# Kernel optimization log

Hardware: AMD Instinct MI355X
Metric: run time of the kernel (lower is better)

The kernel has to match this reference:

```python
import jax, jax.numpy as jnp
import numpy as np

N = 2048; K = 2048; D = 256; D_RESHAPE = 800
HA = 256; DA = 128; HK = 128; HC = 128; HS = 256
S = max(10, int(0.1 * K))  # n_sample = 204
BN_SCALE = 1.0 / float(np.sqrt(1.0 + 1e-5))  # eval BatchNorm1d with running stats (0,1)

def leaky(x):
    return jax.nn.leaky_relu(x, 0.01)

def conv2d(x, w, b):
    y = jax.lax.conv_general_dilated(x, w, (1, 1), 'VALID', dimension_numbers=('NCHW', 'OIHW', 'NCHW'))
    return y + b[None, :, None, None]

def maxpool2(x):
    return jax.lax.reduce_window(x, -jnp.inf, jax.lax.max, (1, 1, 2, 2), (1, 1, 2, 2), 'VALID')

def data_transform(x, c1w, c1b, c2w, c2b, ew, eb):
    h = maxpool2(leaky(conv2d(x, c1w, c1b)))   # [n,20,12,12]
    h = maxpool2(leaky(conv2d(h, c2w, c2b)))   # [n,50,4,4]
    h = h.reshape(-1, D_RESHAPE)
    return leaky(h @ ew.T + eb)                # [n,D]

def skip_block(X, w1, b1, w2, b2, w3, b3):
    # Conv1d kernel_size=1 == per-position linear over channels
    X1 = leaky(X @ w1.T + b1) * BN_SCALE       # [n,HC]
    X2 = leaky(X @ w2.T + b2) * BN_SCALE       # [n,HC]
    X3 = leaky(X @ w3.T + b3) * BN_SCALE       # [n,d]
    feat = jax.nn.softmax(X1 @ X2.T, axis=0)   # torch Softmax(dim=1) on [1,n,n] -> axis 0
    return feat @ X3 + X

def mask_scores(A, w1, b1, w2, b2, w3, b3, w4, b4):
    X1 = leaky(A @ w1.T + b1)                  # [n,HK]
    X2 = jnp.tanh(A @ w2.T + b2)               # [n,HK]
    M = X1.T @ X2                              # [HK,HK]
    A3 = leaky(M @ w3.T + b3)                  # [HK,K]
    s = A3.T @ w4[0] + b4[0]                   # [K]
    return jax.nn.softmax(s)

def attention(X, few, feb, vw, vb, uw, ub, aww, awb, ew, eb):
    H = leaky(X @ few.T + feb)                 # [n,HA]
    AV = jnp.tanh(H @ vw.T + vb)
    AU = leaky(H @ uw.T + ub)
    a = leaky((AV * AU) @ aww.T + awb)         # [n,1]
    A = jax.nn.softmax(a.T, axis=1)            # [1,n]
    M = leaky((A @ H) @ ew.T + eb)             # [1,d]
    return M, A

def euclid(X, Y):
    d2 = jnp.sum(X * X, 1)[:, None] + jnp.sum(Y * Y, 1)[None, :] - 2.0 * (X @ Y.T)
    return jnp.sqrt(jnp.maximum(d2, 0.0))


def setup_inputs() -> dict:
    key = jax.random.key(0)
    ks = iter(jax.random.split(key, 70))
    def rn(shape, scale=0.05):
        return jax.random.normal(next(ks), shape, dtype=jnp.float32) * scale
    d = {}
    d['B'] = jax.random.normal(next(ks), (N, 1, 28, 28), dtype=jnp.float32)
    d['KB'] = jax.random.normal(next(ks), (K, 1, 28, 28), dtype=jnp.float32)
    d['dt_c1_w'] = rn((20, 1, 5, 5)); d['dt_c1_b'] = rn((20,))
    d['dt_c2_w'] = rn((50, 20, 5, 5)); d['dt_c2_b'] = rn((50,))
    d['dt_emb_w'] = rn((D, D_RESHAPE)); d['dt_emb_b'] = rn((D,))
    for nm, dd in (('sk1', D), ('sk2', D), ('sk3', K)):
        d[nm + '_w1'] = rn((HC, dd)); d[nm + '_b1'] = rn((HC,))
        d[nm + '_w2'] = rn((HC, dd)); d[nm + '_b2'] = rn((HC,))
        d[nm + '_w3'] = rn((dd, dd)); d[nm + '_b3'] = rn((dd,))
    d['mk_w1'] = rn((HK, K)); d['mk_b1'] = rn((HK,))
    d['mk_w2'] = rn((HK, K)); d['mk_b2'] = rn((HK,))
    d['mk_w3'] = rn((K, HK)); d['mk_b3'] = rn((K,))
    d['mk_w4'] = rn((1, HK)); d['mk_b4'] = rn((1,))
    d['fuse_w'] = rn((D, D + S)); d['fuse_b'] = rn((D,))
    for nm, din in (('a1', D), ('a2', 2 * D)):
        d[nm + '_fe_w'] = rn((HA, din)); d[nm + '_fe_b'] = rn((HA,))
        d[nm + '_v_w'] = rn((DA, HA)); d[nm + '_v_b'] = rn((DA,))
        d[nm + '_u_w'] = rn((DA, HA)); d[nm + '_u_b'] = rn((DA,))
        d[nm + '_aw_w'] = rn((1, DA)); d[nm + '_aw_b'] = rn((1,))
        d[nm + '_emb_w'] = rn((din, HA)); d[nm + '_emb_b'] = rn((din,))
    d['semb_w'] = rn((HS, 2 * D)); d['semb_b'] = rn((HS,))
    d['cls_w'] = rn((1, HS)); d['cls_b'] = rn((1,))
    return d


def reference(B, KB, dt_c1_w, dt_c1_b, dt_c2_w, dt_c2_b, dt_emb_w, dt_emb_b,
              sk1_w1, sk1_b1, sk1_w2, sk1_b2, sk1_w3, sk1_b3,
              sk2_w1, sk2_b1, sk2_w2, sk2_b2, sk2_w3, sk2_b3,
              sk3_w1, sk3_b1, sk3_w2, sk3_b2, sk3_w3, sk3_b3,
              mk_w1, mk_b1, mk_w2, mk_b2, mk_w3, mk_b3, mk_w4, mk_b4,
              fuse_w, fuse_b,
              a1_fe_w, a1_fe_b, a1_v_w, a1_v_b, a1_u_w, a1_u_b, a1_aw_w, a1_aw_b, a1_emb_w, a1_emb_b,
              a2_fe_w, a2_fe_b, a2_v_w, a2_v_b, a2_u_w, a2_u_b, a2_aw_w, a2_aw_b, a2_emb_w, a2_emb_b,
              semb_w, semb_b, cls_w, cls_b):
    B_dt = data_transform(B, dt_c1_w, dt_c1_b, dt_c2_w, dt_c2_b, dt_emb_w, dt_emb_b)
    KB_dt = data_transform(KB, dt_c1_w, dt_c1_b, dt_c2_w, dt_c2_b, dt_emb_w, dt_emb_b)
    Xs = skip_block(B_dt, sk1_w1, sk1_b1, sk1_w2, sk1_b2, sk1_w3, sk1_b3)
    Ks = skip_block(KB_dt, sk2_w1, sk2_b1, sk2_w2, sk2_b2, sk2_w3, sk2_b3)
    # torch detaches the affinity (.detach().numpy())
    aff = euclid(jax.lax.stop_gradient(Xs), jax.lax.stop_gradient(Ks))  # [N,K]
    aff_s = skip_block(aff, sk3_w1, sk3_b1, sk3_w2, sk3_b2, sk3_w3, sk3_b3)
    scores = mask_scores(aff_s, mk_w1, mk_b1, mk_w2, mk_b2, mk_w3, mk_b3, mk_w4, mk_b4)
    idx = jnp.argsort(-scores)[:S]                       # top-S knowledge columns
    B_bag = jax.nn.softmax(aff_s[:, idx], axis=1)        # [N,S], torch Softmax(dim=2)
    B_fuse = leaky(jnp.concatenate([B_dt, B_bag], axis=1) @ fuse_w.T + fuse_b)  # [N,D]
    M1, _ = attention(B_fuse, a1_fe_w, a1_fe_b, a1_v_w, a1_v_b, a1_u_w, a1_u_b, a1_aw_w, a1_aw_b, a1_emb_w, a1_emb_b)
    X2 = jnp.concatenate([B_fuse, jnp.tile(M1, (B_fuse.shape[0], 1))], axis=1)  # [N,2D]
    bvec, A = attention(X2, a2_fe_w, a2_fe_b, a2_v_w, a2_v_b, a2_u_w, a2_u_b, a2_aw_w, a2_aw_b, a2_emb_w, a2_emb_b)
    bvec = leaky(bvec @ semb_w.T + semb_b)               # [1,HS]
    Y = jnp.clip(jax.nn.sigmoid(bvec @ cls_w.T + cls_b), 1e-5, 1.0 - 1e-5)
    return (Y, A)
```

## Files before the change

### kernel.cpp

```cpp
#include <hip/hip_runtime.h>
#include <math.h>

#define LEAKY(x) ((x) > 0.f ? (x) : 0.01f * (x))
static constexpr float BN_SCALE = 0.9999950000374997f;

typedef unsigned short ushort_t;
typedef float f32x4 __attribute__((ext_vector_type(4)));
typedef short bf16x8 __attribute__((ext_vector_type(8)));

__device__ __forceinline__ ushort_t f2bfu(float f) {
  union { float f; unsigned u; } v; v.f = f;
  unsigned r = v.u + 0x7fffu + ((v.u >> 16) & 1u);
  return (ushort_t)(r >> 16);
}
__device__ __forceinline__ float bfu2f(ushort_t u) {
  union { unsigned u; float f; } v; v.u = ((unsigned)u) << 16;
  return v.f;
}

__device__ __forceinline__ void gload16(const ushort_t* g, ushort_t* lds) {
  __builtin_amdgcn_global_load_lds(
      (const __attribute__((address_space(1))) void*)g,
      (__attribute__((address_space(3))) void*)lds, 16, 0, 0);
}

__global__ void fill_out(float* out, int n) {
  int i = blockIdx.x * 256 + threadIdx.x;
  if (i < n) out[i] = 0.25f;
}

struct CvtArgs {
  const float* src[20];
  ushort_t* dst[20];
  int cum[21];
};
__global__ void to_bf16_flat(CvtArgs a) {
  int total = a.cum[20];
  for (int i = blockIdx.x * 256 + threadIdx.x; i < total; i += gridDim.x * 256) {
    int s = 0;
    while (i >= a.cum[s + 1]) ++s;
    int off = i - a.cum[s];
    a.dst[s][off] = f2bfu(a.src[s][off]);
  }
}

struct BiasPk { const float* a[12]; float* out; };
__global__ void bias_pack(BiasPk p) {
  int b = blockIdx.x, t = threadIdx.x;
  p.out[b * 256 + t] = (t < 128) ? p.a[2 * b][t] : p.a[2 * b + 1][t - 128];
}

__global__ void pad_rows_bf16(const float* __restrict__ w, ushort_t* __restrict__ wp,
                              int O, int Kin, int Kpad) {
  int idx = blockIdx.x * 256 + threadIdx.x;
  if (idx >= O * Kpad) return;
  int o = idx / Kpad, k = idx - o * Kpad;
  wp[idx] = (k < Kin) ? f2bfu(w[(size_t)o * Kin + k]) : (ushort_t)0;
}

__global__ void w2_relayout(const float* __restrict__ w2, ushort_t* __restrict__ w2p) {
  int idx = blockIdx.x * 256 + threadIdx.x;
  if (idx >= 64 * 640) return;
  int oc = idx / 640, k = idx - oc * 640;
  int tap = k / 24, ic = k - tap * 24;
  float v = 0.f;
  if (oc < 50 && tap < 25 && ic < 20)
    v = w2[(size_t)(oc * 20 + ic) * 25 + tap];
  w2p[idx] = f2bfu(v);
}

#define XCD_SWZ(TILE)                                                          \
  int id_ = blockIdx.y * gridDim.x + blockIdx.x;                               \
  int nwg_ = gridDim.x * gridDim.y;                                            \
  int sw_ = (id_ & 7) * (nwg_ >> 3) + (id_ >> 3);                              \
  int bm = (sw_ / gridDim.x) * (TILE), bn = (sw_ % gridDim.x) * (TILE);

__launch_bounds__(256)
__global__ void conv12_mfma(const float* __restrict__ imgB, const float* __restrict__ imgK,
                            const float* __restrict__ w1, const float* __restrict__ b1,
                            const ushort_t* __restrict__ w2p, const float* __restrict__ b2,
                            ushort_t* __restrict__ out832) {
  __shared__ __align__(16) char smem[34816];
  ushort_t* h1T = (ushort_t*)smem;
  ushort_t* Bs  = (ushort_t*)(smem + 13824);
  float* simg = (float*)(smem + 13824);
  float* sw1  = (float*)(smem + 20992);
  float* b1s  = (float*)(smem + 22992);
  float* Cf   = (float*)smem;

  int tid = threadIdx.x;
  int bx = blockIdx.x;
  const float* imgb = (bx < 1024) ? imgB + (size_t)bx * 2 * 784
                                  : imgK + (size_t)(bx - 1024) * 2 * 784;

  for (int i = tid; i < 1568; i += 256) {
    int im = (i >= 784) ? 1 : 0;
    int r = i - im * 784;
    int row = r / 28, col = r - row * 28;
    int sc = (col + (row >> 1)) & 31;
    simg[im * 896 + row * 32 + sc] = imgb[i];
  }
  for (int i = tid; i < 500; i += 256) sw1[i] = w1[i];
  if (tid < 20) b1s[tid] = b1[tid];
  for (int i = tid; i < 288; i += 256) {
    uint2 z; z.x = 0; z.y = 0;
    *(uint2*)&h1T[i * 24 + 20] = z;
  }

  int sB_r = tid >> 2;
  int sB_j0 = (tid & 3) * 2;
  bf16x8 wreg[2];
  #pragma unroll
  for (int i = 0; i < 2; ++i)
    wreg[i] = *(const bf16x8*)&w2p[(size_t)sB_r * 640 + (sB_j0 + i) * 8];

  __syncthreads();

  for (int o = tid; o < 1152; o += 256) {
    int im = (o >= 576) ? 1 : 0;
    int rem = o - im * 576;
    int cg = rem & 3;
    int pos = rem >> 2;
    int py = pos / 12, px = pos - py * 12;
    int y0 = py * 2, x0 = px * 2;
    float p[6][6];
    #pragma unroll
    for (int yy = 0; yy < 6; ++yy) {
      int rr = y0 + yy;
      int rbase = im * 896 + rr * 32;
      int rot = rr >> 1;
      #pragma unroll
      for (int xx = 0; xx < 6; ++xx)
        p[yy][xx] = simg[rbase + ((x0 + xx + rot) & 31)];
    }
    #pragma unroll
    for (int cc = 0; cc < 5; ++cc) {
      int c = cg * 5 + cc;
      const float* wc = &sw1[c * 25];
      float bb = b1s[c];
      float t0 = bb, t1 = bb, t2 = bb, t3 = bb;
      #pragma unroll
      for (int ky = 0; ky < 5; ++ky)
        #pragma unroll
        for (int kx = 0; kx < 5; ++kx) {
          float wv = wc[ky * 5 + kx];
          t0 += p[ky][kx] * wv;
          t1 += p[ky][kx + 1] * wv;
          t2 += p[ky + 1][kx] * wv;
          t3 += p[ky + 1][kx + 1] * wv;
        }
      float mx = fmaxf(fmaxf(t0, t1), fmaxf(t2, t3));
      h1T[(im * 144 + pos) * 24 + c] = f2bfu(LEAKY(mx));
    }
  }

  int wave = tid >> 6, lane = tid & 63;
  int wm = (wave >> 1) * 64, wn = (wave & 1) * 32;
  int mrow = lane & 15, kq = lane >> 4;

  int imv[4], oyv[4], oxv[4];
  #pragma unroll
  for (int mt = 0; mt < 4; ++mt) {
    int r = wm + mt * 16 + mrow;
    imv[mt] = r >> 6;
    int op = r & 63;
    oyv[mt] = op >> 3;
    oxv[mt] = op & 7;
  }

  f32x4 acc[4][2];
  #pragma unroll
  for (int i = 0; i < 4; ++i)
    #pragma unroll
    for (int j = 0; j < 2; ++j)
      #pragma unroll
      for (int r = 0; r < 4; ++r) acc[i][j][r] = 0.f;

  for (int kb = 0; kb < 10; ++kb) {
    __syncthreads();
    #pragma unroll
    for (int i = 0; i < 2; ++i)
      *(bf16x8*)&Bs[sB_r * 72 + (sB_j0 + i) * 8] = wreg[i];
    if (kb + 1 < 10) {
      #pragma unroll
      for (int i = 0; i < 2; ++i)
        wreg[i] = *(const bf16x8*)&w2p[(size_t)sB_r * 640 + (kb + 1) * 64 + (sB_j0 + i) * 8];
    }
    __syncthreads();
    #pragma unroll
    for (int ks = 0; ks < 2; ++ks) {
      int g = kb * 8 + ks * 4 + kq;
      int tap = g / 3;
      int part = g - tap * 3;
      int tc = tap < 25 ? tap : 24;
      int ky = tc / 5, kx = tc - ky * 5;
      bf16x8 af[4], bf[2];
      #pragma unroll
      for (int mt = 0; mt < 4; ++mt) {
        int pos = (oyv[mt] + ky) * 12 + oxv[mt] + kx;
        af[mt] = *(const bf16x8*)&h1T[(imv[mt] * 144 + pos) * 24 + part * 8];
      }
      #pragma unroll
      for (int nt = 0; nt < 2; ++nt)
        bf[nt] = *(const bf16x8*)&Bs[(wn + nt * 16 + mrow) * 72 + ks * 32 + kq * 8];
      #pragma unroll
      for (int mt = 0; mt < 4; ++mt)
        #pragma unroll
        for (int nt = 0; nt < 2; ++nt)
          acc[mt][nt] = __builtin_amdgcn_mfma_f32_16x16x32_bf16(af[mt], bf[nt], acc[mt][nt], 0, 0, 0);
    }
  }
  __syncthreads();
  #pragma unroll
  for (int mt = 0; mt < 4; ++mt)
    #pragma unroll
    for (int nt = 0; nt < 2; ++nt) {
      int n0 = wn + nt * 16 + (lane & 15);
      #pragma unroll
      for (int r = 0; r < 4; ++r)
        Cf[(wm + mt * 16 + kq * 4 + r) * 68 + n0] = acc[mt][nt][r];
    }
  __syncthreads();
  for (int o = tid; o < 1664; o += 256) {
    int im = o / 832, oi = o - im * 832;
    ushort_t val = 0;
    if (oi < 800) {
      int oc = oi >> 4, p = oi & 15, py = p >> 2, px = p & 3;
      int r0 = im * 64 + py * 16 + px * 2;
      float bb = b2[oc];
      float t0 = LEAKY(Cf[r0 * 68 + oc] + bb);
      float t1 = LEAKY(Cf[(r0 + 1) * 68 + oc] + bb);
      float t2 = LEAKY(Cf[(r0 + 8) * 68 + oc] + bb);
      float t3 = LEAKY(Cf[(r0 + 9) * 68 + oc] + bb);
      val = f2bfu(fmaxf(fmaxf(t0, t1), fmaxf(t2, t3)));
    }
    out832[(size_t)(bx * 2 + im) * 832 + oi] = val;
  }
}

enum { EPI_NONE = 0, EPI_LEAKY = 1, EPI_LEAKY_BN = 2, EPI_TANH = 3, EPI_EUCLID = 4,
       EPI_LEAKY_BN_ROW = 5, EPI_RES = 6 };

template <int EPI>
__launch_bounds__(256)
__global__ void gemm_bf16_nt(const ushort_t* __restrict__ A, const ushort_t* __restrict__ B,
                             const float* __restrict__ bias, float* __restrict__ C32,
                             ushort_t* __restrict__ C16, int M, int N, int Kd,
                             const float* __restrict__ e1, const float* __restrict__ e2) {
  __shared__ __align__(16) ushort_t As[2][8192];
  __shared__ __align__(16) ushort_t Bs[2][8192];
  int tid = threadIdx.x;
  XCD_SWZ(128)
  int wave = tid >> 6, lane = tid & 63;
  int wm = (wave >> 1) * 64, wn = (wave & 1) * 64;
  int mrow = lane & 15, kq = lane >> 4;
  int cc[4];
  const ushort_t* ga[4];
  const ushort_t* gb[4];
  #pragma unroll
  for (int q = 0; q < 4; ++q) {
    int c = (wave * 4 + q) * 64 + lane;
    cc[q] = c;
    int row = (c >> 2) & 127, sl = c >> 9, j = c & 3;
    ga[q] = A + (size_t)(bm + row) * Kd + sl * 32 + j * 8;
    gb[q] = B + (size_t)(bn + row) * Kd + sl * 32 + j * 8;
  }

  f32x4 acc[4][4];
  #pragma unroll
  for (int i = 0; i < 4; ++i)
    #pragma unroll
    for (int j = 0; j < 4; ++j)
      #pragma unroll
      for (int r = 0; r < 4; ++r) acc[i][j][r] = 0.f;

  #pragma unroll
  for (int q = 0; q < 4; ++q) {
    gload16(ga[q], &As[0][cc[q] * 8]);
    gload16(gb[q], &Bs[0][cc[q] * 8]);
  }
  int nt = Kd >> 6;
  for (int t = 0; t < nt; ++t) {
    int cur = t & 1;
    __syncthreads();
    if (t + 1 < nt) {
      int ko = (t + 1) * 64;
// ... 209 lines not shown
template <int EPI>
__launch_bounds__(256)
__global__ void gemm_nt64_dual(const ushort_t* __restrict__ A, const ushort_t* __restrict__ B1,
                               const ushort_t* __restrict__ B2, const float* __restrict__ bias1,
                               const float* __restrict__ bias2, ushort_t* __restrict__ C16,
                               int M, int N, int Kd, int Msplit) {
  __shared__ __align__(16) ushort_t As[2][4096];
  __shared__ __align__(16) ushort_t Bs[2][4096];
  int tid = threadIdx.x;
  XCD_SWZ(64)
  const ushort_t* B = (bm < Msplit) ? B1 : B2;
  const float* bias = (bm < Msplit) ? bias1 : bias2;
  GEMM64_PRE(A, B, Kd)
  f32x4 acc[2][2];
  #pragma unroll
  for (int i = 0; i < 2; ++i)
    #pragma unroll
    for (int j = 0; j < 2; ++j)
      #pragma unroll
      for (int r = 0; r < 4; ++r) acc[i][j][r] = 0.f;
  GEMM64_LOOP(Kd)
  #pragma unroll
  for (int mt = 0; mt < 2; ++mt)
    #pragma unroll
    for (int nt2 = 0; nt2 < 2; ++nt2) {
      int n_g = bn + wn + nt2 * 16 + (lane & 15);
      #pragma unroll
      for (int r = 0; r < 4; ++r) {
        int m_g = bm + wm + mt * 16 + kq * 4 + r;
        float v = acc[mt][nt2][r] + bias[n_g];
        if (EPI == EPI_LEAKY) v = LEAKY(v);
        else if (EPI == EPI_LEAKY_BN) { v = LEAKY(v); v *= BN_SCALE; }
        C16[(size_t)m_g * N + n_g] = f2bfu(v);
      }
    }
}

template <int EPI1, int EPI2>
__launch_bounds__(256)
__global__ void gemm_nt64_split(const ushort_t* __restrict__ A, const ushort_t* __restrict__ B,
                                const float* __restrict__ biasPk, float* __restrict__ C32,
                                ushort_t* __restrict__ C16, int M, int N, int Kd, int Nsplit) {
  __shared__ __align__(16) ushort_t As[2][4096];
  __shared__ __align__(16) ushort_t Bs[2][4096];
  int tid = threadIdx.x;
  XCD_SWZ(64)
  GEMM64_PRE(A, B, Kd)
  f32x4 acc[2][2];
  #pragma unroll
  for (int i = 0; i < 2; ++i)
    #pragma unroll
    for (int j = 0; j < 2; ++j)
      #pragma unroll
      for (int r = 0; r < 4; ++r) acc[i][j][r] = 0.f;
  GEMM64_LOOP(Kd)
  #pragma unroll
  for (int mt = 0; mt < 2; ++mt)
    #pragma unroll
    for (int nt2 = 0; nt2 < 2; ++nt2) {
      int n_g = bn + wn + nt2 * 16 + (lane & 15);
      #pragma unroll
      for (int r = 0; r < 4; ++r) {
        int m_g = bm + wm + mt * 16 + kq * 4 + r;
        float v = acc[mt][nt2][r] + biasPk[n_g];
        if (n_g < Nsplit) {
          if (EPI1 == EPI_LEAKY) v = LEAKY(v);
          else if (EPI1 == EPI_TANH) v = tanhf(v);
        } else {
          if (EPI2 == EPI_LEAKY) v = LEAKY(v);
          else if (EPI2 == EPI_TANH) v = tanhf(v);
        }
        if (C32) C32[(size_t)m_g * N + n_g] = v;
        if (C16) C16[(size_t)m_g * N + n_g] = f2bfu(v);
      }
    }
}

__launch_bounds__(256)
__global__ void gemm_w3T_z(const ushort_t* __restrict__ W3a, const ushort_t* __restrict__ W3b,
                           const float* __restrict__ b3a, const float* __restrict__ b3b,
                           const ushort_t* __restrict__ dtb, ushort_t* __restrict__ X3T) {
  const int N = 2048, Kd = 256;
  int z = blockIdx.z;
  const ushort_t* A = z ? W3b : W3a;
  const float* bias = z ? b3b : b3a;
  const ushort_t* B = dtb + (size_t)z * 2048 * 256;
  ushort_t* C = X3T + (size_t)z * 256 * 2048;
  __shared__ __align__(16) ushort_t As[2][4096];
  __shared__ __align__(16) ushort_t Bs[2][4096];
  int tid = threadIdx.x;
  XCD_SWZ(64)
  GEMM64_PRE(A, B, Kd)
  f32x4 acc[2][2];
  #pragma unroll
  for (int i = 0; i < 2; ++i)
    #pragma unroll
    for (int j = 0; j < 2; ++j)
      #pragma unroll
      for (int r = 0; r < 4; ++r) acc[i][j][r] = 0.f;
  GEMM64_LOOP(Kd)
  #pragma unroll
  for (int mt = 0; mt < 2; ++mt)
    #pragma unroll
    for (int nt2 = 0; nt2 < 2; ++nt2) {
      int n_g = bn + wn + nt2 * 16 + (lane & 15);
      #pragma unroll
      for (int r = 0; r < 4; ++r) {
        int m_g = bm + wm + mt * 16 + kq * 4 + r;
        float v = acc[mt][nt2][r] + bias[m_g];
        v = LEAKY(v); v *= BN_SCALE;
        C[(size_t)m_g * N + n_g] = f2bfu(v);
      }
    }
}

__launch_bounds__(256)
__global__ void gemm_ntt_res64_z(const ushort_t* __restrict__ SmatBase,
                                 const ushort_t* __restrict__ X3T,
                                 const ushort_t* __restrict__ dtb,
                                 ushort_t* __restrict__ XsKs) {
  const int N = 256, Kd = 2048;
  int z = blockIdx.z;
  const ushort_t* A = SmatBase + (size_t)z * 2048 * 2048;
  const ushort_t* B = X3T + (size_t)z * 256 * 2048;
  const ushort_t* R = dtb + (size_t)z * 2048 * 256;
  ushort_t* C = XsKs + (size_t)z * 2048 * 256;
  __shared__ __align__(16) ushort_t As[2][4096];
  __shared__ __align__(16) ushort_t Bs[2][4096];
  int tid = threadIdx.x;
  XCD_SWZ(64)
  GEMM64_PRE(A, B, Kd)
  f32x4 acc[2][2];
  #pragma unroll
  for (int i = 0; i < 2; ++i)
    #pragma unroll
    for (int j = 0; j < 2; ++j)
      #pragma unroll
      for (int r = 0; r < 4; ++r) acc[i][j][r] = 0.f;
  GEMM64_LOOP(Kd)
  #pragma unroll
  for (int mt = 0; mt < 2; ++mt)
    #pragma unroll
    for (int nt2 = 0; nt2 < 2; ++nt2) {
      int n_g = bn + wn + nt2 * 16 + (lane & 15);
      #pragma unroll
      for (int r = 0; r < 4; ++r) {
        int m_g = bm + wm + mt * 16 + kq * 4 + r;
        float v = acc[mt][nt2][r] + bfu2f(R[(size_t)m_g * N + n_g]);
        C[(size_t)m_g * N + n_g] = f2bfu(v);
      }
    }
}

__global__ void gemm_tn_part(const ushort_t* __restrict__ X, float* __restrict__ part) {
  int tx = threadIdx.x & 15, ty = threadIdx.x >> 4;
  int i = blockIdx.y * 16 + ty, j = blockIdx.x * 16 + tx;
  int ks = blockIdx.z;
  float acc = 0.f;
  for (int k = ks * 128; k < ks * 128 + 128; ++k)
    acc += bfu2f(X[(size_t)k * 256 + i]) * bfu2f(X[(size_t)k * 256 + 128 + j]);
  part[(size_t)ks * 16384 + i * 128 + j] = acc;
}
__global__ void gemm_tn_reduce(const float* __restrict__ part, ushort_t* __restrict__ Mm) {
  int idx = blockIdx.x * 256 + threadIdx.x;
  float s = 0.f;
  #pragma unroll
  for (int ks = 0; ks < 16; ++ks) s += part[(size_t)ks * 16384 + idx];
  Mm[idx] = f2bfu(s);
}

__global__ void smax_partA(const ushort_t* __restrict__ Sb, float* __restrict__ pm,
                           float* __restrict__ pl, int N) {
  int z = blockIdx.z;
  const ushort_t* S = Sb + (size_t)z * 2048 * 2048;
  int t = threadIdx.x;
  int col = blockIdx.x * 64 + (t & 63);
  int g = t >> 6;
  int r0 = blockIdx.y * 128 + g;
  float vals[32];
  #pragma unroll
  for (int i = 0; i < 32; ++i)
    vals[i] = bfu2f(S[(size_t)(r0 + 4 * i) * N + col]);
  float m = -1e30f;
  #pragma unroll
  for (int i = 0; i < 32; ++i) m = fmaxf(m, vals[i]);
  float l = 0.f;
  #pragma unroll
  for (int i = 0; i < 32; ++i) l += expf(vals[i] - m);
  __shared__ float rm[4][64], rl[4][64];
  rm[g][t & 63] = m; rl[g][t & 63] = l;
  __syncthreads();
  if (g == 0) {
    int c = t & 63;
    float M0 = rm[0][c], L0 = rl[0][c];
    #pragma unroll
    for (int j = 1; j < 4; ++j) {
      float Mj = rm[j][c], Lj = rl[j][c];
      float nm = fmaxf(M0, Mj);
      L0 = L0 * expf(M0 - nm) + Lj * expf(Mj - nm);
      M0 = nm;
    }
    pm[((size_t)z * 16 + blockIdx.y) * N + col] = M0;
    pl[((size_t)z * 16 + blockIdx.y) * N + col] = L0;
  }
}
__global__ void smax_partC(ushort_t* __restrict__ Sb, const float* __restrict__ pm,
                           const float* __restrict__ pl, int N) {
  int z = blockIdx.z;
  ushort_t* S = Sb + (size_t)z * 2048 * 2048;
  int t = threadIdx.x;
  int col = blockIdx.x * 64 + (t & 63);
  int g = t >> 6;
  __shared__ float sgm[64], sgi[64];
  if (t < 64) {
    float m = -1e30f, l = 0.f;
    for (int b = 0; b < 16; ++b) {
      float bm = pm[((size_t)z * 16 + b) * N + col];
      float bl = pl[((size_t)z * 16 + b) * N + col];
      float nm = fmaxf(m, bm);
      l = l * expf(m - nm) + bl * expf(bm - nm);
      m = nm;
    }
    sgm[t] = m;
    sgi[t] = 1.f / l;
  }
  __syncthreads();
  float m = sgm[t & 63], inv = sgi[t & 63];
  int r0 = blockIdx.y * 128 + g;
  #pragma unroll 8
  for (int i = 0; i < 32; ++i) {
    size_t idx = (size_t)(r0 + 4 * i) * N + col;
    S[idx] = f2bfu(expf(bfu2f(S[idx]) - m) * inv);
  }
}

__global__ void row_norm_bf16(const ushort_t* __restrict__ X, float* __restrict__ out, int Kd) {
  int r = blockIdx.x * 2 + (threadIdx.x >> 5);
  int l = threadIdx.x & 31;
  bf16x8 v = *(const bf16x8*)&X[(size_t)r * Kd + l * 8];
  float s = 0.f;
  #pragma unroll
  for (int j = 0; j < 8; ++j) { float f = bfu2f((ushort_t)v[j]); s += f * f; }
  for (int off = 16; off; off >>= 1) s += __shfl_down(s, off, 32);
  if (l == 0) out[r] = s;
}

__global__ void mask_score(const float* __restrict__ A3, const float* __restrict__ w4,
                           const float* __restrict__ b4, float* __restrict__ s) {
  __shared__ float red[4][64];
  int t = threadIdx.x;
  int col = blockIdx.x * 64 + (t & 63);
  int seg = t >> 6;
  float acc = 0.f;
  for (int h = seg * 32; h < seg * 32 + 32; ++h)
    acc += A3[(size_t)h * 2048 + col] * w4[h];
  red[seg][t & 63] = acc;
  __syncthreads();
  if (seg == 0)
    s[col] = red[0][t] + red[1][t] + red[2][t] + red[3][t] + b4[0];
}

__global__ void topk_rank(const float* __restrict__ s, int* __restrict__ idx, int K, int S) {
  __shared__ float sv[2048];
  int t = threadIdx.x;
  for (int i = t; i < K; i += 256) sv[i] = s[i];
  __syncthreads();
  int j = blockIdx.x * 256 + t;
  if (j >= K) return;
  float sj = sv[j];
  int rank = 0;
  #pragma unroll 8
  for (int i = 0; i < 2048; ++i) {
    float si = sv[i];
    rank += (si > sj) || (si == sj && i < j);
  }
  if (rank < S) idx[rank] = j;
}

__global__ void build_cat(const ushort_t* __restrict__ Bdt, const ushort_t* __restrict__ affs,
                          const int* __restrict__ idx, ushort_t* __restrict__ cat) {
  int r = blockIdx.x, t = threadIdx.x;
  __shared__ float vals[256];
  __shared__ float red[256];
  float v = -1e30f;
  if (t < 204) {
    int ix = idx[t];
    ix = ix < 0 ? 0 : (ix > 2047 ? 2047 : ix);
    v = bfu2f(affs[(size_t)r * 2048 + ix]);
  }
  vals[t] = v;
  red[t] = v;
  __syncthreads();
  for (int off = 128; off; off >>= 1) { if (t < off) red[t] = fmaxf(red[t], red[t + off]); __syncthreads(); }
  float m = red[0];
  __syncthreads();
  float e = (t < 204) ? expf(vals[t] - m) : 0.f;
  red[t] = e;
  __syncthreads();
  for (int off = 128; off; off >>= 1) { if (t < off) red[t] += red[t + off]; __syncthreads(); }
  float inv = 1.f / red[0];
  cat[(size_t)r * 512 + t] = Bdt[(size_t)r * 256 + t];
  cat[(size_t)r * 512 + 256 + t] = (t < 204) ? f2bfu(e * inv) : (ushort_t)0;
}

__global__ void attn_gate(const float* __restrict__ AVU, const float* __restrict__ aww,
                          const float* __restrict__ awb, float* __restrict__ a, int n) {
  int wave = threadIdx.x >> 6, lane = threadIdx.x & 63;
  int r = blockIdx.x * 4 + wave;
  if (r >= n) return;
  float s = 0.f;
  #pragma unroll
  for (int j = 0; j < 2; ++j) {
    int d = lane + 64 * j;
    s += AVU[(size_t)r * 256 + d] * AVU[(size_t)r * 256 + 128 + d] * aww[d];
  }
  for (int off = 32; off; off >>= 1) s += __shfl_down(s, off);
  if (lane == 0) {
    float acc = s + awb[0];
    a[r] = LEAKY(acc);
  }
}

__global__ void softmax_vec(const float* __restrict__ x, float* __restrict__ y,
                            float* __restrict__ y2, int n) {
  __shared__ float red[256];
  int t = threadIdx.x;
  float m = -1e30f;
  for (int i = t; i < n; i += 256) m = fmaxf(m, x[i]);
  red[t] = m;
  __syncthreads();
  for (int off = 128; off; off >>= 1) { if (t < off) red[t] = fmaxf(red[t], red[t + off]); __syncthreads(); }
  m = red[0];
  __syncthreads();
  float s = 0.f;
  for (int i = t; i < n; i += 256) s += expf(x[i] - m);
  red[t] = s;
  __syncthreads();
  for (int off = 128; off; off >>= 1) { if (t < off) red[t] += red[t + off]; __syncthreads(); }
  float inv = 1.f / red[0];
  for (int i = t; i < n; i += 256) {
    float v = expf(x[i] - m) * inv;
    y[i] = v;
    if (y2) y2[i] = v;
  }
}

__global__ void colsum_part(const float* __restrict__ wv, const ushort_t* __restrict__ H,
                            float* __restrict__ part, int n) {
  int bk = blockIdx.x, c = threadIdx.x;
  float s = 0.f;
  for (int r = bk; r < n; r += 64) s += wv[r] * bfu2f(H[(size_t)r * 256 + c]);
  part[bk * 256 + c] = s;
}
__global__ void colsum_fin(const float* __restrict__ part, float* __restrict__ out) {
  int c = threadIdx.x;
  float s = 0.f;
  #pragma unroll
  for (int k = 0; k < 64; ++k) s += part[k * 256 + c];
  out[c] = s;
}

__global__ void gemv_act(const float* __restrict__ x, const float* __restrict__ W,
                         const float* __restrict__ b, float* __restrict__ out,
                         int O, int Kd, int act) {
  int wave = threadIdx.x >> 6, lane = threadIdx.x & 63;
  int o = blockIdx.x * 4 + wave;
  if (o >= O) return;
  float s = 0.f;
  for (int c = lane; c < Kd; c += 64) s += x[c] * W[(size_t)o * Kd + c];
  for (int off = 32; off; off >>= 1) s += __shfl_down(s, off);
  if (lane == 0) {
    float acc = s + (b ? b[o] : 0.f);
    out[o] = act ? LEAKY(acc) : acc;
  }
}

__global__ void build_cat2(const ushort_t* __restrict__ Bf, const float* __restrict__ M1,
                           ushort_t* __restrict__ cat2) {
  int r = blockIdx.x, t = threadIdx.x;
  cat2[(size_t)r * 512 + t] = (t < 256) ? Bf[(size_t)r * 256 + t] : f2bfu(M1[t - 256]);
}

__global__ void final_head(const float* __restrict__ AH2, const float* __restrict__ embw,
                           const float* __restrict__ embb, const float* __restrict__ sembw,
                           const float* __restrict__ sembb, const float* __restrict__ clsw,
                           const float* __restrict__ clsb, float* __restrict__ Yout) {
  __shared__ float sAH[256];
  __shared__ float bvec[512];
  __shared__ float prod[256];
  int t = threadIdx.x;
  int wave = t >> 6, lane = t & 63;
  if (t < 256) sAH[t] = AH2[t];
  __syncthreads();
  for (int i = 0; i < 64; ++i) {
    int o = wave * 64 + i;
    float s = 0.f;
    #pragma unroll
    for (int j = 0; j < 4; ++j) {
      int c = lane + 64 * j;
      s += sAH[c] * embw[(size_t)o * 256 + c];
    }
    for (int off = 32; off; off >>= 1) s += __shfl_down(s, off);
    if (lane == 0) bvec[o] = LEAKY(s + embb[o]);
  }
  __syncthreads();
  for (int i = 0; i < 32; ++i) {
    int o = wave * 32 + i;
    float s = 0.f;
    #pragma unroll
    for (int j = 0; j < 8; ++j) {
      int c = lane + 64 * j;
      s += bvec[c] * sembw[(size_t)o * 512 + c];
    }
    for (int off = 32; off; off >>= 1) s += __shfl_down(s, off);
    if (lane == 0) {
      float a2 = LEAKY(s + sembb[o]);
      prod[o] = a2 * clsw[o];
    }
  }
  __syncthreads();
  if (t < 64) {
    float s = prod[t] + prod[t + 64] + prod[t + 128] + prod[t + 192];
    for (int off = 32; off; off >>= 1) s += __shfl_down(s, off);
    if (t == 0) {
      float y = s + clsb[0];
      y = 1.f / (1.f + expf(-y));
      y = fminf(fmaxf(y, 1e-5f), 1.f - 1e-5f);
      Yout[0] = y;
    }
  }
}

extern "C" void kernel_launch(void* const* d_in, const int* in_sizes, int n_in,
                              void* d_out, int out_size, void* d_ws, size_t ws_size,
                              hipStream_t stream) {
  auto IN = [&](int i) { return (const float*)d_in[i]; };
  (void)n_in; (void)in_sizes; (void)out_size;

  const int S = 204;
  float* out_f = (float*)d_out;

  float* W = (float*)d_ws;
  size_t off = 0;
  auto F = [&](size_t n) { float* p = W + off; off += n; return p; };
  auto FU = [&](size_t nus) { return (ushort_t*)F((nus + 1) / 2); };

  ushort_t* dt_b  = FU((size_t)4096 * 256);
  ushort_t* XsKs  = FU((size_t)4096 * 256);
  ushort_t* X12b  = FU((size_t)4096 * 256);
  ushort_t* X3sb  = FU((size_t)4096 * 256);
  ushort_t* aff_b = FU((size_t)2048 * 2048);
  float* AVU   = F((size_t)2048 * 256);
  ushort_t* Mm_b = FU((size_t)128 * 128);
  float* svec  = F(2048);
  int*   idxb  = (int*)F(256);
  float* avec  = F(2048);
  float* Awv   = F(2048);
  float* AH    = F(256);
  float* M1v   = F(256);
  float* AH2   = F(256);
  float* nxy   = F(4096);
  float* part  = F(16384);
  float* sm_pm = F((size_t)2 * 16 * 2048);
  float* sm_pl = F((size_t)2 * 16 * 2048);
  float* pbias = F(6 * 256);

  size_t wo = 0;
  ushort_t* warena = (ushort_t*)F(3250000);
  auto WA = [&](size_t n) { ushort_t* p = warena + wo; wo = (wo + n + 15) & ~(size_t)15; return p; };
  ushort_t* w2p   = WA(40960);
  ushort_t* embp  = WA(212992);
  ushort_t* s1w1 = WA(32768); ushort_t* s1w2 = WA(32768); ushort_t* s1w3 = WA(65536);
  ushort_t* s2w1 = WA(32768); ushort_t* s2w2 = WA(32768); ushort_t* s2w3 = WA(65536);
  ushort_t* s3w1 = WA(262144); ushort_t* s3w2 = WA(262144); ushort_t* s3w3 = WA(4194304);
  ushort_t* mw1 = WA(262144); ushort_t* mw2 = WA(262144); ushort_t* mw3 = WA(262144);
  ushort_t* fwp = WA(131072);
  ushort_t* a1fe = WA(65536); ushort_t* a1v = WA(32768); ushort_t* a1u = WA(32768);
  ushort_t* a2fe = WA(131072); ushort_t* a2v = WA(32768); ushort_t* a2u = WA(32768);
  (void)s1w2; (void)s2w2; (void)s3w2; (void)mw2; (void)a1u; (void)a2u;

  float* pool = F((size_t)4194304);

  const size_t NEED_BYTES = off * 4;
  if (ws_size < NEED_BYTES) {
    fill_out<<<9, 256, 0, stream>>>(out_f, 2049);
    return;
  }

  ushort_t* h2h_b   = (ushort_t*)pool;
  ushort_t* SmatB   = (ushort_t*)pool;
  ushort_t* X3b_b   = (ushort_t*)(pool + 2097152);
  float* A3   = pool;
  float* tnpt = pool + 262144;
  ushort_t* cat_b   = (ushort_t*)pool;
  ushort_t* cat2_b  = (ushort_t*)(pool + 524288);
  ushort_t* Bfuse_b = (ushort_t*)(pool + 1048576);
  ushort_t* Hbuf_b  = (ushort_t*)(pool + 1310720);

  CvtArgs ca;
  const float* srcs[20] = { IN(6), IN(8), IN(10), IN(12), IN(14), IN(16), IN(18),
                            IN(20), IN(22), IN(24), IN(26), IN(28), IN(30),
                            IN(36), IN(38), IN(40), IN(46), IN(48), IN(50), IN(4) };
  ushort_t* dsts[20] = { nullptr, s1w1, s1w2, s1w3, s2w1, s2w2, s2w3,
                         s3w1, s3w2, s3w3, mw1, mw2, mw3,
                         a1fe, a1v, a1u, a2fe, a2v, a2u, w2p };
  int lens[20] = { 0, 32768, 32768, 65536, 32768, 32768, 65536,
                   262144, 262144, 4194304, 262144, 262144, 262144,
                   65536, 32768, 32768, 131072, 32768, 32768, 0 };
  int cum = 0;
  for (int i = 0; i < 20; ++i) {
    ca.src[i] = srcs[i]; ca.dst[i] = dsts[i] ? dsts[i] : w2p;
    ca.cum[i] = cum; cum += lens[i];
  }
  ca.cum[20] = cum;
  to_bf16_flat<<<2048, 256, 0, stream>>>(ca);
  w2_relayout<<<160, 256, 0, stream>>>(IN(4), w2p);
  pad_rows_bf16<<<512, 256, 0, stream>>>(IN(34), fwp, 256, 460, 512);
  pad_rows_bf16<<<832, 256, 0, stream>>>(IN(6), embp, 256, 800, 832);
  BiasPk bp;
  const float* bsrc[12] = { IN(9), IN(11), IN(15), IN(17), IN(21), IN(23),
                            IN(27), IN(29), IN(39), IN(41), IN(49), IN(51) };
  for (int i = 0; i < 12; ++i) bp.a[i] = bsrc[i];
  bp.out = pbias;
  bias_pack<<<6, 256, 0, stream>>>(bp);
  float* pb_sk1 = pbias, *pb_sk2 = pbias + 256, *pb_sk3 = pbias + 512;
  float* pb_msk = pbias + 768, *pb_a1 = pbias + 1024, *pb_a2 = pbias + 1280;

  conv12_mfma<<<2048, 256, 0, stream>>>(IN(0), IN(1), IN(2), IN(3), w2p, IN(5), h2h_b);
  gemm_bf16_nt64<EPI_LEAKY><<<dim3(4, 64), 256, 0, stream>>>(
      h2h_b, embp, IN(7), nullptr, dt_b, 4096, 256, 832);

  gemm_nt64_dual<EPI_LEAKY_BN><<<dim3(4, 64), 256, 0, stream>>>(
      dt_b, s1w1, s2w1, pb_sk1, pb_sk2, X12b, 4096, 256, 256, 2048);
  gemm_w3T_z<<<dim3(32, 4, 2), 256, 0, stream>>>(s1w3, s2w3, IN(13), IN(19), dt_b, X3sb);
  gemm_smat_z<<<dim3(16, 16, 2), 256, 0, stream>>>(X12b, SmatB);
  smax_partA<<<dim3(32, 16, 2), 256, 0, stream>>>(SmatB, sm_pm, sm_pl, 2048);
  smax_partC<<<dim3(32, 16, 2), 256, 0, stream>>>(SmatB, sm_pm, sm_pl, 2048);
  gemm_ntt_res64_z<<<dim3(4, 32, 2), 256, 0, stream>>>(SmatB, X3sb, dt_b, XsKs);

  row_norm_bf16<<<2048, 64, 0, stream>>>(XsKs, nxy, 256);
  gemm_bf16_nt<EPI_EUCLID><<<dim3(16, 16), 256, 0, stream>>>(
      XsKs, XsKs + (size_t)2048 * 256, nullptr, nullptr, aff_b, 2048, 2048, 256,
      nxy, nxy + 2048);

  gemm_bf16_nt64<EPI_LEAKY_BN><<<dim3(4, 32), 256, 0, stream>>>(
      aff_b, s3w1, pb_sk3, nullptr, X12b, 2048, 256, 2048);
  gemm_smat_z<<<dim3(16, 16, 1), 256, 0, stream>>>(X12b, SmatB);
  gemm_bf16_nt<EPI_LEAKY_BN_ROW><<<dim3(16, 16), 256, 0, stream>>>(
      s3w3, aff_b, IN(25), nullptr, X3b_b, 2048, 2048, 2048, nullptr, nullptr);
  smax_partA<<<dim3(32, 16, 1), 256, 0, stream>>>(SmatB, sm_pm, sm_pl, 2048);
  smax_partC<<<dim3(32, 16, 1), 256, 0, stream>>>(SmatB, sm_pm, sm_pl, 2048);
  gemm_bf16_nt<EPI_RES><<<dim3(16, 16), 256, 0, stream>>>(
      SmatB, X3b_b, nullptr, nullptr, aff_b, 2048, 2048, 2048,
      (const float*)aff_b, nullptr);
  ushort_t* affs_b = aff_b;

  gemm_nt64_split<EPI_LEAKY, EPI_TANH><<<dim3(4, 32), 256, 0, stream>>>(
      affs_b, mw1, pb_msk, nullptr, X12b, 2048, 256, 2048, 128);
  gemm_tn_part<<<dim3(8, 8, 16), 256, 0, stream>>>(X12b, tnpt);
  gemm_tn_reduce<<<64, 256, 0, stream>>>(tnpt, Mm_b);
  gemm_bf16_nt64<EPI_LEAKY><<<dim3(32, 2), 256, 0, stream>>>(
      Mm_b, mw3, IN(31), A3, nullptr, 128, 2048, 128);
  mask_score<<<32, 256, 0, stream>>>(A3, IN(32), IN(33), svec);
  topk_rank<<<8, 256, 0, stream>>>(svec, idxb, 2048, S);

  build_cat<<<2048, 256, 0, stream>>>(dt_b, affs_b, idxb, cat_b);
  gemm_bf16_nt64<EPI_LEAKY><<<dim3(4, 32), 256, 0, stream>>>(
      cat_b, fwp, IN(35), nullptr, Bfuse_b, 2048, 256, 512);

  gemm_bf16_nt64<EPI_LEAKY><<<dim3(4, 32), 256, 0, stream>>>(
      Bfuse_b, a1fe, IN(37), nullptr, Hbuf_b, 2048, 256, 256);
  gemm_nt64_split<EPI_TANH, EPI_LEAKY><<<dim3(4, 32), 256, 0, stream>>>(
      Hbuf_b, a1v, pb_a1, AVU, nullptr, 2048, 256, 256, 128);
  attn_gate<<<512, 256, 0, stream>>>(AVU, IN(42), IN(43), avec, 2048);
  softmax_vec<<<1, 256, 0, stream>>>(avec, Awv, nullptr, 2048);
  colsum_part<<<64, 256, 0, stream>>>(Awv, Hbuf_b, part, 2048);
  colsum_fin<<<1, 256, 0, stream>>>(part, AH);
  gemv_act<<<64, 256, 0, stream>>>(AH, IN(44), IN(45), M1v, 256, 256, 1);
  build_cat2<<<2048, 512, 0, stream>>>(Bfuse_b, M1v, cat2_b);

  gemm_bf16_nt64<EPI_LEAKY><<<dim3(4, 32), 256, 0, stream>>>(
      cat2_b, a2fe, IN(47), nullptr, Hbuf_b, 2048, 256, 512);
  gemm_nt64_split<EPI_TANH, EPI_LEAKY><<<dim3(4, 32), 256, 0, stream>>>(
      Hbuf_b, a2v, pb_a2, AVU, nullptr, 2048, 256, 256, 128);
  attn_gate<<<512, 256, 0, stream>>>(AVU, IN(52), IN(53), avec, 2048);
  softmax_vec<<<1, 256, 0, stream>>>(avec, Awv, out_f + 1, 2048);
  colsum_part<<<64, 256, 0, stream>>>(Awv, Hbuf_b, part, 2048);
  colsum_fin<<<1, 256, 0, stream>>>(part, AH2);

  final_head<<<1, 512, 0, stream>>>(AH2, IN(54), IN(55), IN(56), IN(57),
                                    IN(58), IN(59), out_f);
}
```

Baseline: 810.1 us.

## Fuse M1 concat into fe2 GEMM and softmax into colsum, drop image swizzle

Adds a dedicated gemm_fe2 kernel that reads the Bfuse rows and a broadcast M1 vector directly for its second K-half, so the build_cat2 kernel and the [N,512] concat buffer are no longer needed. The attention softmax is folded into the weighted column-sum kernel: each block recomputes max and sum over the 2048 gate values, which removes a single-block softmax launch but repeats the reduction in every block. The conv1 image staging also drops its rotated LDS layout for a plain row layout, which may bring back LDS bank conflicts in exchange for simpler addressing.

```diff
diff --git a/kernel.cpp b/kernel.cpp
--- a/kernel.cpp
+++ b/kernel.cpp
@@ -97,8 +97,7 @@
     int im = (i >= 784) ? 1 : 0;
     int r = i - im * 784;
     int row = r / 28, col = r - row * 28;
-    int sc = (col + (row >> 1)) & 31;
-    simg[im * 896 + row * 32 + sc] = imgb[i];
+    simg[im * 896 + row * 32 + col] = imgb[i];
   }
   for (int i = tid; i < 500; i += 256) sw1[i] = w1[i];
   if (tid < 20) b1s[tid] = b1[tid];
@@ -126,12 +125,10 @@
     float p[6][6];
     #pragma unroll
     for (int yy = 0; yy < 6; ++yy) {
-      int rr = y0 + yy;
-      int rbase = im * 896 + rr * 32;
-      int rot = rr >> 1;
+      const float* rb = &simg[im * 896 + (y0 + yy) * 32 + x0];
       #pragma unroll
       for (int xx = 0; xx < 6; ++xx)
-        p[yy][xx] = simg[rbase + ((x0 + xx + rot) & 31)];
+        p[yy][xx] = rb[xx];
     }
     #pragma unroll
     for (int cc = 0; cc < 5; ++cc) {
@@ -647,6 +644,83 @@
     }
 }
 
+__launch_bounds__(256)
+__global__ void gemm_fe2(const ushort_t* __restrict__ Bf, const ushort_t* __restrict__ M1b,
+                         const ushort_t* __restrict__ Bw, const float* __restrict__ bias,
+                         ushort_t* __restrict__ C16) {
+  const int N = 256, Kd = 512;
+  __shared__ __align__(16) ushort_t As[2][4096];
+  __shared__ __align__(16) ushort_t Bs[2][4096];
+  int tid = threadIdx.x;
+  XCD_SWZ(64)
+  int wave = tid >> 6, lane = tid & 63;
+  int wm = (wave >> 1) * 32, wn = (wave & 1) * 32;
+  int mrow = lane & 15, kq = lane >> 4;
+  int c0 = wave * 128 + lane;
+  int c1 = c0 + 64;
+  int r0_ = (c0 >> 2) & 63, off0 = (c0 >> 8) * 32 + (c0 & 3) * 8;
+  int r1_ = (c1 >> 2) & 63, off1 = (c1 >> 8) * 32 + (c1 & 3) * 8;
+  const ushort_t* gb0 = Bw + (size_t)(bn + r0_) * Kd + off0;
+  const ushort_t* gb1 = Bw + (size_t)(bn + r1_) * Kd + off1;
+
+  f32x4 acc[2][2];
+  #pragma unroll
+  for (int i = 0; i < 2; ++i)
+    #pragma unroll
+    for (int j = 0; j < 2; ++j)
+      #pragma unroll
+      for (int r = 0; r < 4; ++r) acc[i][j][r] = 0.f;
+
+  gload16(Bf + (size_t)(bm + r0_) * 256 + off0, &As[0][c0 * 8]);
+  gload16(Bf + (size_t)(bm + r1_) * 256 + off1, &As[0][c1 * 8]);
+  gload16(gb0, &Bs[0][c0 * 8]);
+  gload16(gb1, &Bs[0][c1 * 8]);
+  for (int t = 0; t < 8; ++t) {
+    int cur = t & 1;
+    __syncthreads();
+    if (t + 1 < 8) {
+      int tn = t + 1;
+      int ko = tn * 64;
+      const ushort_t* a0 = (tn < 4) ? Bf + (size_t)(bm + r0_) * 256 + ko + off0
+                                    : M1b + (ko - 256) + off0;
+      const ushort_t* a1 = (tn < 4) ? Bf + (size_t)(bm + r1_) * 256 + ko + off1
+                                    : M1b + (ko - 256) + off1;
+      gload16(a0, &As[cur ^ 1][c0 * 8]);
+      gload16(a1, &As[cur ^ 1][c1 * 8]);
+      gload16(gb0 + ko, &Bs[cur ^ 1][c0 * 8]);
+      gload16(gb1 + ko, &Bs[cur ^ 1][c1 * 8]);
+    }
+    #pragma unroll
+    for (int ks = 0; ks < 2; ++ks) {
+      bf16x8 af[2], bf[2];
+      #pragma unroll
+      for (int mt = 0; mt < 2; ++mt)
+        af[mt] = *(const bf16x8*)&As[cur][ks * 2048 + (wm + mt * 16 + mrow) * 32 + kq * 8];
+      #pragma unroll
+      for (int nt2 = 0; nt2 < 2; ++nt2)
+        bf[nt2] = *(const bf16x8*)&Bs[cur][ks * 2048 + (wn + nt2 * 16 + mrow) * 32 + kq * 8];
+      #pragma unroll
+      for (int mt = 0; mt < 2; ++mt)
+        #pragma unroll
+        for (int nt2 = 0; nt2 < 2; ++nt2)
+          acc[mt][nt2] = __builtin_amdgcn_mfma_f32_16x16x32_bf16(af[mt], bf[nt2], acc[mt][nt2], 0, 0, 0);
+    }
+  }
+  #pragma unroll
+  for (int mt = 0; mt < 2; ++mt)
+    #pragma unroll
+    for (int nt2 = 0; nt2 < 2; ++nt2) {
+      int n_g = bn + wn + nt2 * 16 + (lane & 15);
+      #pragma unroll
+      for (int r = 0; r < 4; ++r) {
+        int m_g = bm + wm + mt * 16 + kq * 4 + r;
+        float v = acc[mt][nt2][r] + bias[n_g];
+        v = LEAKY(v);
+        C16[(size_t)m_g * N + n_g] = f2bfu(v);
+      }
+    }
+}
+
 __global__ void gemm_tn_part(const ushort_t* __restrict__ X, float* __restrict__ part) {
   int tx = threadIdx.x & 15, ty = threadIdx.x >> 4;
   int i = blockIdx.y * 16 + ty, j = blockIdx.x * 16 + tx;
@@ -816,8 +890,7 @@
   }
 }
 
-__global__ void softmax_vec(const float* __restrict__ x, float* __restrict__ y,
-                            float* __restrict__ y2, int n) {
+__global__ void softmax_out(const float* __restrict__ x, float* __restrict__ y2, int n) {
   __shared__ float red[256];
   int t = threadIdx.x;
   float m = -1e30f;
@@ -833,19 +906,32 @@
   __syncthreads();
   for (int off = 128; off; off >>= 1) { if (t < off) red[t] += red[t + off]; __syncthreads(); }
   float inv = 1.f / red[0];
-  for (int i = t; i < n; i += 256) {
-    float v = expf(x[i] - m) * inv;
-    y[i] = v;
-    if (y2) y2[i] = v;
-  }
-}
-
-__global__ void colsum_part(const float* __restrict__ wv, const ushort_t* __restrict__ H,
-                            float* __restrict__ part, int n) {
-  int bk = blockIdx.x, c = threadIdx.x;
+  for (int i = t; i < n; i += 256)
+    y2[i] = expf(x[i] - m) * inv;
+}
+
+__global__ void colsum_sm(const float* __restrict__ avec, const ushort_t* __restrict__ H,
+                          float* __restrict__ part, int n) {
+  __shared__ float red[256];
+  int t = threadIdx.x;
+  float m = -1e30f;
+  for (int i = t; i < n; i += 256) m = fmaxf(m, avec[i]);
+  red[t] = m;
+  __syncthreads();
+  for (int off = 128; off; off >>= 1) { if (t < off) red[t] = fmaxf(red[t], red[t + off]); __syncthreads(); }
+  m = red[0];
+  __syncthreads();
   float s = 0.f;
-  for (int r = bk; r < n; r += 64) s += wv[r] * bfu2f(H[(size_t)r * 256 + c]);
-  part[bk * 256 + c] = s;
+  for (int i = t; i < n; i += 256) s += expf(avec[i] - m);
+  red[t] = s;
+  __syncthreads();
+  for (int off = 128; off; off >>= 1) { if (t < off) red[t] += red[t + off]; __syncthreads(); }
+  float inv = 1.f / red[0];
+  int bk = blockIdx.x, c = t;
+  float acc = 0.f;
+  for (int r = bk; r < n; r += 64)
+    acc += expf(avec[r] - m) * inv * bfu2f(H[(size_t)r * 256 + c]);
+  part[bk * 256 + c] = acc;
 }
 __global__ void colsum_fin(const float* __restrict__ part, float* __restrict__ out) {
   int c = threadIdx.x;
@@ -857,7 +943,7 @@
 
 __global__ void gemv_act(const float* __restrict__ x, const float* __restrict__ W,
                          const float* __restrict__ b, float* __restrict__ out,
-                         int O, int Kd, int act) {
+                         ushort_t* __restrict__ out16, int O, int Kd, int act) {
   int wave = threadIdx.x >> 6, lane = threadIdx.x & 63;
   int o = blockIdx.x * 4 + wave;
   if (o >= O) return;
@@ -866,14 +952,10 @@
   for (int off = 32; off; off >>= 1) s += __shfl_down(s, off);
   if (lane == 0) {
     float acc = s + (b ? b[o] : 0.f);
-    out[o] = act ? LEAKY(acc) : acc;
-  }
-}
-
-__global__ void build_cat2(const ushort_t* __restrict__ Bf, const float* __restrict__ M1,
-                           ushort_t* __restrict__ cat2) {
-  int r = blockIdx.x, t = threadIdx.x;
-  cat2[(size_t)r * 512 + t] = (t < 256) ? Bf[(size_t)r * 256 + t] : f2bfu(M1[t - 256]);
+    float v = act ? LEAKY(acc) : acc;
+    out[o] = v;
+    if (out16) out16[o] = f2bfu(v);
+  }
 }
 
 __global__ void final_head(const float* __restrict__ AH2, const float* __restrict__ embw,
@@ -947,10 +1029,10 @@
   ushort_t* aff_b = FU((size_t)2048 * 2048);
   float* AVU   = F((size_t)2048 * 256);
   ushort_t* Mm_b = FU((size_t)128 * 128);
+  ushort_t* M1b  = FU(256);
   float* svec  = F(2048);
   int*   idxb  = (int*)F(256);
   float* avec  = F(2048);
-  float* Awv   = F(2048);
   float* AH    = F(256);
   float* M1v   = F(256);
   float* AH2   = F(256);
@@ -988,7 +1070,6 @@
   float* A3   = pool;
   float* tnpt = pool + 262144;
   ushort_t* cat_b   = (ushort_t*)pool;
-  ushort_t* cat2_b  = (ushort_t*)(pool + 524288);
   ushort_t* Bfuse_b = (ushort_t*)(pool + 1048576);
   ushort_t* Hbuf_b  = (ushort_t*)(pool + 1310720);
 
@@ -1068,19 +1149,16 @@
   gemm_nt64_split<EPI_TANH, EPI_LEAKY><<<dim3(4, 32), 256, 0, stream>>>(
       Hbuf_b, a1v, pb_a1, AVU, nullptr, 2048, 256, 256, 128);
   attn_gate<<<512, 256, 0, stream>>>(AVU, IN(42), IN(43), avec, 2048);
-  softmax_vec<<<1, 256, 0, stream>>>(avec, Awv, nullptr, 2048);
-  colsum_part<<<64, 256, 0, stream>>>(Awv, Hbuf_b, part, 2048);
+  colsum_sm<<<64, 256, 0, stream>>>(avec, Hbuf_b, part, 2048);
   colsum_fin<<<1, 256, 0, stream>>>(part, AH);
-  gemv_act<<<64, 256, 0, stream>>>(AH, IN(44), IN(45), M1v, 256, 256, 1);
-  build_cat2<<<2048, 512, 0, stream>>>(Bfuse_b, M1v, cat2_b);
-
-  gemm_bf16_nt64<EPI_LEAKY><<<dim3(4, 32), 256, 0, stream>>>(
-      cat2_b, a2fe, IN(47), nullptr, Hbuf_b, 2048, 256, 512);
+  gemv_act<<<64, 256, 0, stream>>>(AH, IN(44), IN(45), M1v, M1b, 256, 256, 1);
+
+  gemm_fe2<<<dim3(4, 32), 256, 0, stream>>>(Bfuse_b, M1b, a2fe, IN(47), Hbuf_b);
   gemm_nt64_split<EPI_TANH, EPI_LEAKY><<<dim3(4, 32), 256, 0, stream>>>(
       Hbuf_b, a2v, pb_a2, AVU, nullptr, 2048, 256, 256, 128);
   attn_gate<<<512, 256, 0, stream>>>(AVU, IN(52), IN(53), avec, 2048);
-  softmax_vec<<<1, 256, 0, stream>>>(avec, Awv, out_f + 1, 2048);
-  colsum_part<<<64, 256, 0, stream>>>(Awv, Hbuf_b, part, 2048);
+  softmax_out<<<1, 256, 0, stream>>>(avec, out_f + 1, 2048);
+  colsum_sm<<<64, 256, 0, stream>>>(avec, Hbuf_b, part, 2048);
   colsum_fin<<<1, 256, 0, stream>>>(part, AH2);
 
   final_head<<<1, 512, 0, stream>>>(AH2, IN(54), IN(55), IN(56), IN(57),
```

After: 805.5 us. Within noise of the previous version (-0.6%).
